# Performance work log

Hardware: AMD Instinct MI355X
Metric: run time of the kernel (lower is better)

## Reference

```python
import jax, jax.numpy as jnp
import numpy as np

B, C, D = 4096, 128, 768
EPS = 1e-12
SEP = 4.0  # pair_dist in [0, 2], so 4.0 separates per-class key bands


def setup_inputs() -> dict:
    key = jax.random.key(0)
    k1, k2, k3, k4 = jax.random.split(key, 4)
    features = jax.random.normal(k1, (B, D), jnp.float32)
    centers = jax.random.normal(k2, (C, D), jnp.float32)
    labels = jax.random.randint(k3, (B,), 0, C, dtype=jnp.int32)
    cam_ids = jax.random.randint(k4, (B,), 0, 8, dtype=jnp.int32)
    return {"features": features, "centers": centers, "labels": labels, "cam_ids": cam_ids}


def _l2norm(x):
    return x / jnp.maximum(jnp.linalg.norm(x, axis=1, keepdims=True), EPS)


def reference(features, centers, labels, cam_ids):
    # cam_ids is unused by the original module.
    E = _l2norm(features)                         # [B, D] unit embeddings
    Cn = _l2norm(jax.lax.stop_gradient(centers))  # [C, D] unit centers (detached)

    S = E @ E.T                                   # [B, B] pairwise cosine (differentiable)
    EC = jnp.sum(E * Cn[labels], axis=1)          # [B] cosine(embedding_i, center_{label_i})

    li = labels[:, None]
    lj = labels[None, :]
    ar = jnp.arange(B)
    upper = ar[:, None] < ar[None, :]             # i < j (each unordered pair once)
    valid = (li == lj) & upper                    # within-class pairs

    # pair distances are computed under no_grad in torch -> stop_gradient
    pd = jax.lax.stop_gradient(1.0 - jnp.clip(S, -1.0, 1.0))  # [B, B]

    # per-class lower-median threshold via ONE global sort:
    # key = class_id * SEP + pair_dist groups pairs by class, sorted by dist within class
    m = jnp.zeros((C,), jnp.int32).at[labels].add(1)   # class sizes
    npairs = (m * (m - 1)) // 2                         # pairs per class
    key_mat = jnp.where(valid, li.astype(jnp.float32) * SEP + pd, jnp.inf)
    sorted_keys = jnp.sort(key_mat.ravel())             # [B*B]
    offs = jnp.cumsum(npairs) - npairs                  # start of each class segment
    med_idx = offs + jnp.maximum(npairs - 1, 0) // 2    # torch.median = lower median
    thr = sorted_keys[med_idx] - SEP * jnp.arange(C, dtype=jnp.float32)
    thr = jnp.where(npairs > 0, thr, jnp.inf)           # classes with <2 samples: no pairs

    sel = valid & (pd > thr[labels][:, None])           # strict > as in torch

    # random interpolation ratio (no_grad in torch)
    r = jax.lax.stop_gradient(jax.random.uniform(jax.random.key(1), (B, B), jnp.float32))

    # sampled = normalize(r*e_i + (1-r)*e_j); since ||e||=1:
    #   ||sampled_pre||^2 = r^2 + (1-r)^2 + 2 r (1-r) <e_i, e_j>
    #   <sampled, c> = (r <e_i,c> + (1-r) <e_j,c>) / ||sampled_pre||
    norm2 = r * r + (1.0 - r) * (1.0 - r) + 2.0 * r * (1.0 - r) * S
    norm = jnp.maximum(jnp.sqrt(jnp.maximum(norm2, 0.0)), EPS)
    dot = (r * EC[:, None] + (1.0 - r) * EC[None, :]) / norm
    dist = 1.0 - jnp.clip(dot, -1.0, 1.0)               # [B, B]

    # the torch loop iterates over every label occurrence, so a class with m_c
    # occurrences contributes its class loss (and pair count) m_c times
    w = m[labels].astype(jnp.float32)[:, None]          # weight per pair (left label's class)
    loss = jnp.sum(jnp.where(sel, w * dist, 0.0))
    nsamp = jnp.sum(jnp.where(sel, w, 0.0))
    return jnp.where(nsamp > 0, loss / nsamp, 0.0)
```

## Files before the change

### kernel.cpp

```cpp
#include <hip/hip_runtime.h>

#define B_ 4096
#define C_ 128
#define D_ 768
#define NT 1024
#define NW (NT/64)
#define M_MAX 96
#define P_MAX (M_MAX*(M_MAX-1)/2)
#define CK 128
#define NCH (D_/CK)
#define SROW 132
#define TILE_F (M_MAX*SROW)
#define LM2 2
#define RC 127
#define SPT ((M_MAX*(CK/4) + NT - 1)/NT)

__device__ __forceinline__ float wave_red(float v){
#pragma unroll
  for (int o = 32; o > 0; o >>= 1) v += __shfl_down(v, o, 64);
  return v;
}
__device__ __forceinline__ float wave_min(float v){
#pragma unroll
  for (int o = 32; o > 0; o >>= 1) v = fminf(v, __shfl_down(v, o, 64));
  return v;
}
__device__ __forceinline__ float wave_max(float v){
#pragma unroll
  for (int o = 32; o > 0; o >>= 1) v = fmaxf(v, __shfl_down(v, o, 64));
  return v;
}
__device__ __forceinline__ float clamp1(float x){ return fminf(fmaxf(x, -1.f), 1.f); }
__device__ __forceinline__ unsigned rotl32(unsigned x, int r){ return (x << r) | (x >> (32 - r)); }
__device__ __forceinline__ float dot4(float4 a, float4 b){
  return fmaf(a.x, b.x, fmaf(a.y, b.y, fmaf(a.z, b.z, a.w * b.w)));
}

__device__ float rand_ij(unsigned n){
  const unsigned half = (unsigned)B_ * (unsigned)B_ / 2u;
  unsigned c0, c1; bool hi;
  if (n < half){ c0 = n; c1 = n + half; hi = false; }
  else         { c0 = n - half; c1 = n; hi = true; }
  const unsigned K0 = 0u, K1 = 1u, K2 = 0x1BD11BDBu;
  unsigned x0 = c0 + K0, x1 = c1 + K1;
#define TFR(r) { x0 += x1; x1 = rotl32(x1, (r)); x1 ^= x0; }
  TFR(13) TFR(15) TFR(26) TFR(6)  x0 += K1; x1 += K2 + 1u;
  TFR(17) TFR(29) TFR(16) TFR(24) x0 += K2; x1 += K0 + 2u;
  TFR(13) TFR(15) TFR(26) TFR(6)  x0 += K0; x1 += K1 + 3u;
  TFR(17) TFR(29) TFR(16) TFR(24) x0 += K1; x1 += K2 + 4u;
  TFR(13) TFR(15) TFR(26) TFR(6)  x0 += K2; x1 += K0 + 5u;
#undef TFR
  unsigned bits = hi ? x1 : x0;
  return __uint_as_float((bits >> 9) | 0x3F800000u) - 1.0f;
}

__device__ __forceinline__ void decode_pair(int p, int m, int* a_, int* b_){
  float fm = (float)(2*m - 1);
  int a = (int)((fm - sqrtf(fm*fm - 8.0f*(float)p)) * 0.5f);
  a = max(0, min(a, m - 2));
  while (a > 0 && (a*(2*m - 1 - a))/2 > p) --a;
  while (((a + 1)*(2*m - 2 - a))/2 <= p) ++a;
  *a_ = a;
  *b_ = a + 1 + (p - (a*(2*m - 1 - a))/2);
}

__device__ float dotg(const float* x, const float* y){
  float s = 0.f;
  for (int k = 0; k < D_; ++k) s = fmaf(x[k], y[k], s);
  return s;
}
__device__ float S_pair_g(const float* feat, int ga, int gb){
  const float* ra = feat + (size_t)ga * D_;
  const float* rb = feat + (size_t)gb * D_;
  float d = dotg(ra, rb);
  float na = 1.f / fmaxf(sqrtf(dotg(ra, ra)), 1e-12f);
  float nb = 1.f / fmaxf(sqrtf(dotg(rb, rb)), 1e-12f);
  return d * na * nb;
}

__global__ __launch_bounds__(NT) void k_all(
    const float* __restrict__ feat, const float* __restrict__ cent,
    const int* __restrict__ labels,
    float* __restrict__ lossv, float* __restrict__ wv,
    unsigned* __restrict__ flags, float* __restrict__ out)
{
  const int c = blockIdx.x;
  const int tid = threadIdx.x;
  const int wid = tid >> 6, lane = tid & 63;

  __shared__ int   gid_s[M_MAX];
  __shared__ int   mcount;
  __shared__ __align__(16) float tile[2 * TILE_F];
  __shared__ __align__(16) float cvec[2][CK];
  float*          Sl     = tile;
  float*          Pd     = tile + P_MAX;
  unsigned short* fidx_s = (unsigned short*)(tile + 2 * P_MAX);
  __shared__ float selfs[M_MAX];
  __shared__ float ecs[M_MAX];
  __shared__ float cn_sh;
  __shared__ int   wcnt[NW * 64];
  __shared__ float mnb[NW], mxb[NW];
  __shared__ float lo_sh, sF_sh;
  __shared__ int   B0_sh, ex_sh, B1_sh;
  __shared__ float thr_sh;
  __shared__ float redbuf[2 * NW];
  __shared__ int   last_sh;

  if (tid == 0) mcount = 0;
  __syncthreads();
  {
    const int4* lab4 = (const int4*)labels;
    for (int i = tid; i < B_ / 4; i += NT){
      int4 L = lab4[i];
      int base = i << 2;
      if (L.x == c){ int p = atomicAdd(&mcount, 1); if (p < M_MAX) gid_s[p] = base; }
      if (L.y == c){ int p = atomicAdd(&mcount, 1); if (p < M_MAX) gid_s[p] = base + 1; }
      if (L.z == c){ int p = atomicAdd(&mcount, 1); if (p < M_MAX) gid_s[p] = base + 2; }
      if (L.w == c){ int p = atomicAdd(&mcount, 1); if (p < M_MAX) gid_s[p] = base + 3; }
    }
  }
  __syncthreads();
  const int m = mcount;

  float lloss = 0.f, lw = 0.f;

  if (m >= 2 && m <= M_MAX){
    const int P = m * (m - 1) / 2;
    const int k0 = (P - 1) >> 1;
    const float wc = (float)m;
    const int nst = m * (CK / 4);

    const int h    = (m + 1) >> 1;
    const int Upair = h * (h + 1) / 2;
    const int hec  = (m + 2) >> 1;
    const int U    = Upair + hec;

    int c0[LM2], c1[LM2], c2[LM2], c3[LM2];
    int tAv[LM2], tBv[LM2];
    float acc[LM2][4];
    int nlay = 0;
#pragma unroll
    for (int t = 0; t < LM2; ++t){
      acc[t][0] = acc[t][1] = acc[t][2] = acc[t][3] = 0.f;
      c0[t] = c1[t] = c2[t] = c3[t] = 0; tAv[t] = 0; tBv[t] = -3;
      int u = tid + t * NT;
      if (u < U){
        nlay = t + 1;
        if (u < Upair){
          int ta = 0;
          while ((ta + 1) * h - ((ta + 1) * ta) / 2 <= u) ++ta;
          int tb = ta + (u - (ta * h - (ta * (ta - 1)) / 2));
          c0[t] = ta; c1[t] = ta + h; c2[t] = tb; c3[t] = tb + h;
          tAv[t] = ta; tBv[t] = tb;
        } else {
          int g = u - Upair;
          int l1 = g + hec;
          c0[t] = g;
          c1[t] = (l1 == m) ? RC : ((l1 < m) ? l1 : 0);
          c2[t] = RC; c3[t] = RC;
          tAv[t] = g; tBv[t] = -1;
        }
      }
    }

    float4 pf[SPT];
    float4 cpf;
#pragma unroll
    for (int k = 0; k < SPT; ++k){
      int e = tid + k * NT;
      if (e < nst){
        int r = e >> 5, j = e & 31;
        pf[k] = ((const float4*)(feat + (size_t)gid_s[r] * D_))[j];
      }
    }
    if (tid < CK/4) cpf = ((const float4*)(cent + (size_t)c * D_))[tid];
#pragma unroll
    for (int k = 0; k < SPT; ++k){
      int e = tid + k * NT;
      if (e < nst){
        int r = e >> 5, j = e & 31;
        ((float4*)&tile[r * SROW])[j] = pf[k];
      }
    }
    if (tid < CK/4) ((float4*)cvec[0])[tid] = cpf;
    __syncthreads();

    for (int ch = 0; ch < NCH; ++ch){
      const int cur = ch & 1;
      if (ch + 1 < NCH){
        const int d0 = (ch + 1) * CK;
#pragma unroll
        for (int k = 0; k < SPT; ++k){
          int e = tid + k * NT;
          if (e < nst){
            int r = e >> 5, j = e & 31;
            pf[k] = ((const float4*)(feat + (size_t)gid_s[r] * D_ + d0))[j];
          }
        }
        if (tid < CK/4) cpf = ((const float4*)(cent + (size_t)c * D_ + d0))[tid];
      }
      {
        const float* tl = tile + cur * TILE_F;
        const float4* cv4 = (const float4*)cvec[cur];
#pragma unroll
        for (int t = 0; t < LM2; ++t){
          if (t < nlay){
            const float4* A0 = (c0[t] == RC) ? cv4 : (const float4*)&tl[c0[t] * SROW];
            const float4* A1 = (c1[t] == RC) ? cv4 : (const float4*)&tl[c1[t] * SROW];
            const float4* Bp0 = (c2[t] == RC) ? cv4 : (const float4*)&tl[c2[t] * SROW];
            const float4* Bp1 = (c3[t] == RC) ? cv4 : (const float4*)&tl[c3[t] * SROW];
            float s00 = 0.f, s01 = 0.f, s10 = 0.f, s11 = 0.f;
#pragma unroll 8
            for (int j = 0; j < CK/4; ++j){
              float4 a0 = A0[j], a1 = A1[j], b0 = Bp0[j], b1 = Bp1[j];
              s00 += dot4(a0, b0); s01 += dot4(a0, b1);
              s10 += dot4(a1, b0); s11 += dot4(a1, b1);
            }
            acc[t][0] += s00; acc[t][1] += s01;
            acc[t][2] += s10; acc[t][3] += s11;
          }
        }
      }
      if (ch + 1 < NCH){
        float* tn = tile + (cur ^ 1) * TILE_F;
#pragma unroll
        for (int k = 0; k < SPT; ++k){
          int e = tid + k * NT;
          if (e < nst){
            int r = e >> 5, j = e & 31;
            ((float4*)&tn[r * SROW])[j] = pf[k];
          }
        }
        if (tid < CK/4) ((float4*)cvec[cur ^ 1])[tid] = cpf;
      }
      __syncthreads();
    }

#pragma unroll
    for (int t = 0; t < LM2; ++t){
      if (t < nlay){
        if (tBv[t] == -1){
          int g = tAv[t], l1 = g + hec;
          ecs[g] = acc[t][0];
          if (l1 == m) cn_sh = acc[t][2];
          else if (l1 < m) ecs[l1] = acc[t][2];
        } else if (tBv[t] >= 0){
          const int ta = tAv[t], tb = tBv[t];
          const int a1 = ta + h, b1 = tb + h;
          if (ta == tb){
            if (ta < m) selfs[ta] = acc[t][0];
            if (a1 < m) selfs[a1] = acc[t][3];
            if (b1 < m) Sl[(ta*(2*m - 1 - ta))/2 + (b1 - ta - 1)] = acc[t][1];
          } else {
            Sl[(ta*(2*m - 1 - ta))/2 + (tb - ta - 1)] = acc[t][0];
            if (b1 < m) Sl[(ta*(2*m - 1 - ta))/2 + (b1 - ta - 1)] = acc[t][1];
            if (a1 < m) Sl[(tb*(2*m - 1 - tb))/2 + (a1 - tb - 1)] = acc[t][2];
            if (a1 < m && b1 < m) Sl[(a1*(2*m - 1 - a1))/2 + (b1 - a1 - 1)] = acc[t][3];
          }
        }
      }
    }
    __syncthreads();
    if (tid < m){
      float rn  = 1.f / fmaxf(sqrtf(selfs[tid]), 1e-12f);
      float cno = 1.f / fmaxf(sqrtf(cn_sh), 1e-12f);
      selfs[tid] = rn;
      ecs[tid] = ecs[tid] * rn * cno;
    }
    __syncthreads();

    float pmn = 1e30f, pmx = -1e30f;
    for (int p = tid; p < P; p += NT){
      int a, b; decode_pair(p, m, &a, &b);
      float S = Sl[p] * selfs[a] * selfs[b];
      float pd = 1.f - clamp1(S);
      Sl[p] = S; Pd[p] = pd;
      pmn = fminf(pmn, pd); pmx = fmaxf(pmx, pd);
    }
    pmn = wave_min(pmn); pmx = wave_max(pmx);
    if (lane == 0){ mnb[wid] = pmn; mxb[wid] = pmx; }
    __syncthreads();
    if (tid == 0){
      float mn = mnb[0], mx = mxb[0];
#pragma unroll
      for (int i = 1; i < NW; ++i){ mn = fminf(mn, mnb[i]); mx = fmaxf(mx, mxb[i]); }
      lo_sh = mn;
      sF_sh = 4096.f / fmaxf(mx - mn, 1e-20f);
    }
    __syncthreads();
    const float lo = lo_sh, sF = sF_sh;

    const int nch = (P + NT - 1) / NT;
    int cl = 0;
    for (int t = 0; t < nch; ++t){
      int p = tid + t * NT;
      int bkt = -1;
      if (p < P){
        int f = (int)((Pd[p] - lo) * sF);
        f = max(0, min(4095, f));
        fidx_s[p] = (unsigned short)f;
        bkt = f >> 6;
      }
#pragma unroll
      for (int k = 0; k < 64; ++k){
        unsigned long long msk = __ballot(bkt == k);
        if (lane == k) cl += __popcll(msk);
      }
    }
    wcnt[wid*64 + lane] = cl;
    __syncthreads();
    if (tid < 64){
      int tot = 0;
#pragma unroll
      for (int w = 0; w < NW; ++w) tot += wcnt[w*64 + tid];
      int inc = tot;
#pragma unroll
      for (int o = 1; o < 64; o <<= 1){
        int v = __shfl_up(inc, o, 64);
        if (tid >= o) inc += v;
      }
      int excl = inc - tot;
      if (excl <= k0 && k0 < inc){ B0_sh = tid; ex_sh = excl; }
    }
    __syncthreads();
    const int Bsel0 = B0_sh;
    const int kt = k0 - ex_sh;
    cl = 0;
    for (int t = 0; t < nch; ++t){
      int p = tid + t * NT;
      int bkt = -1;
      if (p < P){
        int f = fidx_s[p];
        if ((f >> 6) == Bsel0) bkt = f & 63;
      }
#pragma unroll
      for (int k = 0; k < 64; ++k){
        unsigned long long msk = __ballot(bkt == k);
        if (lane == k) cl += __popcll(msk);
      }
    }
    wcnt[wid*64 + lane] = cl;
    __syncthreads();
    if (tid < 64){
      int tot = 0;
#pragma unroll
      for (int w = 0; w < NW; ++w) tot += wcnt[w*64 + tid];
      int inc = tot;
#pragma unroll
      for (int o = 1; o < 64; o <<= 1){
        int v = __shfl_up(inc, o, 64);
        if (tid >= o) inc += v;
      }
      int excl = inc - tot;
      if (excl <= kt && kt < inc) B1_sh = tid;
    }
    __syncthreads();
    const int fsel = (Bsel0 << 6) | B1_sh;

    {
      const float4* Pd4 = (const float4*)Pd;
      const int nq4 = P >> 2;
      for (int p = tid; p < P; p += NT){
        if (fidx_s[p] == (unsigned short)fsel){
          const float pdp = Pd[p];
          int lt = 0, eq = 0;
#pragma unroll 4
          for (int q4 = 0; q4 < nq4; ++q4){
            float4 v = Pd4[q4];
            lt += (v.x < pdp) + (v.y < pdp) + (v.z < pdp) + (v.w < pdp);
            eq += (v.x == pdp) + (v.y == pdp) + (v.z == pdp) + (v.w == pdp);
          }
          for (int q = nq4 << 2; q < P; ++q){
            float pdq = Pd[q];
            lt += (pdq < pdp); eq += (pdq == pdp);
          }
          if (lt <= k0 && k0 < lt + eq) thr_sh = pdp;
        }
      }
    }
    __syncthreads();
    const float thr = thr_sh;

    for (int p = tid; p < P; p += NT){
      float pd = Pd[p];
      if (pd > thr){
        float S = Sl[p];
        int a, b; decode_pair(p, m, &a, &b);
        int ga = gid_s[a], gb = gid_s[b];
        float ea = ecs[a], eb = ecs[b];
        int i, j; float eci, ecj;
        if (ga < gb){ i = ga; j = gb; eci = ea; ecj = eb; }
        else        { i = gb; j = ga; eci = eb; ecj = ea; }
        float r = rand_ij((unsigned)i * (unsigned)B_ + (unsigned)j);
        float omr = 1.f - r;
        float n2 = r * r + omr * omr + 2.f * r * omr * S;
        float nrm = fmaxf(sqrtf(fmaxf(n2, 0.f)), 1e-12f);
        float dt = clamp1((r * eci + omr * ecj) / nrm);
        lloss += wc * (1.f - dt);
        lw += wc;
      }
    }
  } else if (m > M_MAX){
    int* mem = (int*)Sl;
    if (tid == 0) B0_sh = 0;
    __syncthreads();
    for (int i = tid; i < B_; i += NT)
      if (labels[i] == c){ int p = atomicAdd(&B0_sh, 1); mem[p] = i; }
    __syncthreads();
    const int P = m * (m - 1) / 2;
    const int k0 = (P - 1) >> 1;
    const float wc = (float)m;
    const float* cc = cent + (size_t)c * D_;
    const float cno = 1.f / fmaxf(sqrtf(dotg(cc, cc)), 1e-12f);
    for (int p = tid; p < P; p += NT){
      int a, b; decode_pair(p, m, &a, &b);
      float pdp = 1.f - clamp1(S_pair_g(feat, mem[a], mem[b]));
      int lt = 0, eq = 0;
      for (int q = 0; q < P; ++q){
        int a2, b2; decode_pair(q, m, &a2, &b2);
        float pdq = 1.f - clamp1(S_pair_g(feat, mem[a2], mem[b2]));
        lt += (pdq < pdp); eq += (pdq == pdp);
      }
      if (lt <= k0 && k0 < lt + eq) thr_sh = pdp;
    }
    __syncthreads();
    const float thr = thr_sh;
    for (int p = tid; p < P; p += NT){
      int a, b; decode_pair(p, m, &a, &b);
      int ga = mem[a], gb = mem[b];
      float S = S_pair_g(feat, ga, gb);
      float pd = 1.f - clamp1(S);
      if (pd > thr){
        if (ga > gb){ int t2 = ga; ga = gb; gb = t2; }
        const float* ra = feat + (size_t)ga * D_;
        const float* rb = feat + (size_t)gb * D_;
        float eci = dotg(ra, cc) / fmaxf(sqrtf(dotg(ra, ra)), 1e-12f) * cno;
        float ecj = dotg(rb, cc) / fmaxf(sqrtf(dotg(rb, rb)), 1e-12f) * cno;
        float r = rand_ij((unsigned)ga * (unsigned)B_ + (unsigned)gb);
        float omr = 1.f - r;
        float n2 = r * r + omr * omr + 2.f * r * omr * S;
        float nrm = fmaxf(sqrtf(fmaxf(n2, 0.f)), 1e-12f);
        float dt = clamp1((r * eci + omr * ecj) / nrm);
        lloss += wc * (1.f - dt);
        lw += wc;
      }
    }
  }

  lloss = wave_red(lloss); lw = wave_red(lw);
  if (lane == 0){ redbuf[wid] = lloss; redbuf[NW + wid] = lw; }
  __syncthreads();
  if (tid == 0){
    float tl = 0.f, tw = 0.f;
#pragma unroll
    for (int i = 0; i < NW; ++i){ tl += redbuf[i]; tw += redbuf[NW + i]; }
    __hip_atomic_store(&lossv[c], tl, __ATOMIC_RELAXED, __HIP_MEMORY_SCOPE_AGENT);
    __hip_atomic_store(&wv[c],   tw, __ATOMIC_RELAXED, __HIP_MEMORY_SCOPE_AGENT);
    unsigned old = __hip_atomic_fetch_add(&flags[0], 1u, __ATOMIC_ACQ_REL,
                                          __HIP_MEMORY_SCOPE_AGENT);
    last_sh = ((old & 127u) == 127u) ? 1 : 0;
  }
  __syncthreads();
  if (last_sh){
    float lv = 0.f, wvv = 0.f;
    if (tid < C_){
      lv  = __hip_atomic_load(&lossv[tid], __ATOMIC_RELAXED, __HIP_MEMORY_SCOPE_AGENT);
      wvv = __hip_atomic_load(&wv[tid],   __ATOMIC_RELAXED, __HIP_MEMORY_SCOPE_AGENT);
    }
    lv = wave_red(lv); wvv = wave_red(wvv);
    if (lane == 0){ redbuf[wid] = lv; redbuf[NW + wid] = wvv; }
    __syncthreads();
    if (tid == 0){
      float l = redbuf[0] + redbuf[1];
      float w = redbuf[NW] + redbuf[NW + 1];
      out[0] = (w > 0.f) ? (l / w) : 0.f;
    }
  }
}

extern "C" void kernel_launch(void* const* d_in, const int* in_sizes, int n_in,
                              void* d_out, int out_size, void* d_ws, size_t ws_size,
                              hipStream_t stream)
{
  const float* feat   = (const float*)d_in[0];
  const float* cent   = (const float*)d_in[1];
  const int*   labels = (const int*)d_in[2];

  char* ws = (char*)d_ws;
  float*    lossv = (float*)(ws + 0);
  float*    wvv   = (float*)(ws + 512);
  unsigned* flags = (unsigned*)(ws + 1024);

  k_all<<<C_, NT, 0, stream>>>(feat, cent, labels, lossv, wvv, flags, (float*)d_out);
}
```

Baseline: 128.6 us.

## Fuse pair normalization into accumulator epilogue and use fixed-range bucketing for median select

Pair distances are now normalized and bucketed directly from the GEMM accumulators in registers, so the separate pass over Sl that recomputed S, stored Pd and ran a min/max reduction (plus two barriers) is gone. Bucketing uses a fixed range of [0,2] scaled to 4096 bins instead of a data-dependent min/max range. The final rank search gathers the few candidates in the selected bin into a small shared list and ranks them only against each other, falling back to a full O(P) scan when the list overflows. This cuts shared-memory traffic and the quadratic candidate scan, but with a fixed range, clustered distances may crowd one bin and trigger the slow fallback.

```diff
diff --git a/kernel.cpp b/kernel.cpp
--- a/kernel.cpp
+++ b/kernel.cpp
@@ -14,20 +14,11 @@
 #define LM2 2
 #define RC 127
 #define SPT ((M_MAX*(CK/4) + NT - 1)/NT)
+#define LCAP 64
 
 __device__ __forceinline__ float wave_red(float v){
 #pragma unroll
   for (int o = 32; o > 0; o >>= 1) v += __shfl_down(v, o, 64);
-  return v;
-}
-__device__ __forceinline__ float wave_min(float v){
-#pragma unroll
-  for (int o = 32; o > 0; o >>= 1) v = fminf(v, __shfl_down(v, o, 64));
-  return v;
-}
-__device__ __forceinline__ float wave_max(float v){
-#pragma unroll
-  for (int o = 32; o > 0; o >>= 1) v = fmaxf(v, __shfl_down(v, o, 64));
   return v;
 }
 __device__ __forceinline__ float clamp1(float x){ return fminf(fmaxf(x, -1.f), 1.f); }
@@ -93,16 +84,15 @@
   __shared__ __align__(16) float tile[2 * TILE_F];
   __shared__ __align__(16) float cvec[2][CK];
   float*          Sl     = tile;
-  float*          Pd     = tile + P_MAX;
-  unsigned short* fidx_s = (unsigned short*)(tile + 2 * P_MAX);
+  unsigned short* fidx_s = (unsigned short*)(tile + P_MAX);
   __shared__ float selfs[M_MAX];
   __shared__ float ecs[M_MAX];
   __shared__ float cn_sh;
   __shared__ int   wcnt[NW * 64];
-  __shared__ float mnb[NW], mxb[NW];
-  __shared__ float lo_sh, sF_sh;
-  __shared__ int   B0_sh, ex_sh, B1_sh;
+  __shared__ int   B0_sh, ex_sh, B1_sh, ex2_sh;
   __shared__ float thr_sh;
+  __shared__ float lst[LCAP];
+  __shared__ int   listn;
   __shared__ float redbuf[2 * NW];
   __shared__ int   last_sh;
 
@@ -246,21 +236,16 @@
           else if (l1 < m) ecs[l1] = acc[t][2];
         } else if (tBv[t] >= 0){
           const int ta = tAv[t], tb = tBv[t];
-          const int a1 = ta + h, b1 = tb + h;
+          const int a1 = ta + h;
           if (ta == tb){
             if (ta < m) selfs[ta] = acc[t][0];
             if (a1 < m) selfs[a1] = acc[t][3];
-            if (b1 < m) Sl[(ta*(2*m - 1 - ta))/2 + (b1 - ta - 1)] = acc[t][1];
-          } else {
-            Sl[(ta*(2*m - 1 - ta))/2 + (tb - ta - 1)] = acc[t][0];
-            if (b1 < m) Sl[(ta*(2*m - 1 - ta))/2 + (b1 - ta - 1)] = acc[t][1];
-            if (a1 < m) Sl[(tb*(2*m - 1 - tb))/2 + (a1 - tb - 1)] = acc[t][2];
-            if (a1 < m && b1 < m) Sl[(a1*(2*m - 1 - a1))/2 + (b1 - a1 - 1)] = acc[t][3];
-          }
-        }
-      }
-    }
-    __syncthreads();
+          }
+        }
+      }
+    }
+    __syncthreads();
+    if (tid == 0) listn = 0;
     if (tid < m){
       float rn  = 1.f / fmaxf(sqrtf(selfs[tid]), 1e-12f);
       float cno = 1.f / fmaxf(sqrtf(cn_sh), 1e-12f);
@@ -269,38 +254,40 @@
     }
     __syncthreads();
 
-    float pmn = 1e30f, pmx = -1e30f;
-    for (int p = tid; p < P; p += NT){
-      int a, b; decode_pair(p, m, &a, &b);
-      float S = Sl[p] * selfs[a] * selfs[b];
-      float pd = 1.f - clamp1(S);
-      Sl[p] = S; Pd[p] = pd;
-      pmn = fminf(pmn, pd); pmx = fmaxf(pmx, pd);
-    }
-    pmn = wave_min(pmn); pmx = wave_max(pmx);
-    if (lane == 0){ mnb[wid] = pmn; mxb[wid] = pmx; }
-    __syncthreads();
-    if (tid == 0){
-      float mn = mnb[0], mx = mxb[0];
-#pragma unroll
-      for (int i = 1; i < NW; ++i){ mn = fminf(mn, mnb[i]); mx = fmaxf(mx, mxb[i]); }
-      lo_sh = mn;
-      sF_sh = 4096.f / fmaxf(mx - mn, 1e-20f);
-    }
-    __syncthreads();
-    const float lo = lo_sh, sF = sF_sh;
+    float pdq_[LM2][4];
+    int   fq_[LM2][4];
+#pragma unroll
+    for (int t = 0; t < LM2; ++t){
+#pragma unroll
+      for (int s = 0; s < 4; ++s){ pdq_[t][s] = 0.f; fq_[t][s] = -1; }
+      if (t < nlay && tBv[t] >= 0){
+        const int ta = tAv[t], tb = tBv[t], a1 = ta + h, b1 = tb + h;
+        const int  pa[4]  = { ta, ta, tb, a1 };
+        const int  pb[4]  = { tb, b1, a1, b1 };
+        const bool dif    = (ta != tb);
+        const bool val[4] = { dif, b1 < m, dif && (a1 < m), dif && (a1 < m) && (b1 < m) };
+#pragma unroll
+        for (int s = 0; s < 4; ++s){
+          if (val[s]){
+            float S = acc[t][s] * selfs[pa[s]]; S *= selfs[pb[s]];
+            float pd = 1.f - clamp1(S);
+            int p = (pa[s] * (2*m - 1 - pa[s])) / 2 + (pb[s] - pa[s] - 1);
+            Sl[p] = S;
+            int f = min(4095, (int)(pd * 2048.f));
+            fidx_s[p] = (unsigned short)f;
+            pdq_[t][s] = pd; fq_[t][s] = f;
+          }
+        }
+      }
+    }
+    __syncthreads();
 
     const int nch = (P + NT - 1) / NT;
     int cl = 0;
     for (int t = 0; t < nch; ++t){
       int p = tid + t * NT;
       int bkt = -1;
-      if (p < P){
-        int f = (int)((Pd[p] - lo) * sF);
-        f = max(0, min(4095, f));
-        fidx_s[p] = (unsigned short)f;
-        bkt = f >> 6;
-      }
+      if (p < P) bkt = fidx_s[p] >> 6;
 #pragma unroll
       for (int k = 0; k < 64; ++k){
         unsigned long long msk = __ballot(bkt == k);
@@ -352,26 +339,41 @@
         if (tid >= o) inc += v;
       }
       int excl = inc - tot;
-      if (excl <= kt && kt < inc) B1_sh = tid;
+      if (excl <= kt && kt < inc){ B1_sh = tid; ex2_sh = excl; }
     }
     __syncthreads();
     const int fsel = (Bsel0 << 6) | B1_sh;
-
-    {
-      const float4* Pd4 = (const float4*)Pd;
-      const int nq4 = P >> 2;
+    const int ktf  = kt - ex2_sh;
+
+#pragma unroll
+    for (int t = 0; t < LM2; ++t){
+#pragma unroll
+      for (int s = 0; s < 4; ++s){
+        if (fq_[t][s] == fsel){
+          int ix = atomicAdd(&listn, 1);
+          if (ix < LCAP) lst[ix] = pdq_[t][s];
+        }
+      }
+    }
+    __syncthreads();
+    const int ln = listn;
+    if (ln <= LCAP){
+      if (tid < ln){
+        float pdp = lst[tid];
+        int lt = 0, eq = 0;
+        for (int j = 0; j < ln; ++j){
+          float v = lst[j];
+          lt += (v < pdp); eq += (v == pdp);
+        }
+        if (lt <= ktf && ktf < lt + eq) thr_sh = pdp;
+      }
+    } else {
       for (int p = tid; p < P; p += NT){
         if (fidx_s[p] == (unsigned short)fsel){
-          const float pdp = Pd[p];
+          float pdp = 1.f - clamp1(Sl[p]);
           int lt = 0, eq = 0;
-#pragma unroll 4
-          for (int q4 = 0; q4 < nq4; ++q4){
-            float4 v = Pd4[q4];
-            lt += (v.x < pdp) + (v.y < pdp) + (v.z < pdp) + (v.w < pdp);
-            eq += (v.x == pdp) + (v.y == pdp) + (v.z == pdp) + (v.w == pdp);
-          }
-          for (int q = nq4 << 2; q < P; ++q){
-            float pdq = Pd[q];
+          for (int q = 0; q < P; ++q){
+            float pdq = 1.f - clamp1(Sl[q]);
             lt += (pdq < pdp); eq += (pdq == pdp);
           }
           if (lt <= k0 && k0 < lt + eq) thr_sh = pdp;
@@ -382,9 +384,9 @@
     const float thr = thr_sh;
 
     for (int p = tid; p < P; p += NT){
-      float pd = Pd[p];
+      float S = Sl[p];
+      float pd = 1.f - clamp1(S);
       if (pd > thr){
-        float S = Sl[p];
         int a, b; decode_pair(p, m, &a, &b);
         int ga = gid_s[a], gb = gid_s[b];
         float ea = ecs[a], eb = ecs[b];
```

After: 112.9 us. 12.2% less time.
